# Optimization experiments

Hardware: AMD Instinct MI355X
Metric: run time of the kernel (lower is better)

The kernel has to match this reference:

```python
import jax, jax.numpy as jnp
import numpy as np
from itertools import permutations

NODE, BATCH, DIM, STEP = 32, 64, 32, 8
E = NODE * (NODE - 1)          # 992 directed edges (all ordered pairs)
K = 3                          # edge types
MSG_HID = 64; MSG_OUT = 64; N_HID = 64; PRED_LEN = 8


def setup_inputs() -> dict:
    key = jax.random.key(0)
    ks = jax.random.split(key, 12)
    es = jnp.asarray(np.array(list(permutations(range(NODE), 2))).T, dtype=jnp.int32)  # [2, E]
    x = jax.random.normal(ks[0], (BATCH, NODE, DIM, STEP), jnp.float32)
    z = jax.nn.softmax(jax.random.normal(ks[1], (BATCH, E, K), jnp.float32), axis=-1)
    p = lambda k, shape: jax.random.normal(k, shape, jnp.float32) * 0.1
    return dict(
        x=x, z=z, es=es,
        nodes_mask=jnp.zeros((NODE,), jnp.float32),
        edges_mask=jnp.zeros((E,), jnp.float32),
        mask=jnp.zeros((1,), jnp.float32),
        msg_W1=p(ks[2], (K, 2 * DIM, MSG_HID)), msg_b1=jnp.zeros((K, MSG_HID), jnp.float32),
        msg_W2=p(ks[3], (K, MSG_HID, MSG_OUT)), msg_b2=jnp.zeros((K, MSG_OUT), jnp.float32),
        out_W1=p(ks[4], (DIM + MSG_OUT, N_HID)), out_b1=jnp.zeros((N_HID,), jnp.float32),
        out_W2=p(ks[5], (N_HID, N_HID)), out_b2=jnp.zeros((N_HID,), jnp.float32),
        out_W3=p(ks[6], (N_HID, DIM)), out_b3=jnp.zeros((DIM,), jnp.float32),
        ge_Wi=p(ks[7], (3, N_HID, N_HID)), ge_bi=jnp.zeros((3, N_HID), jnp.float32),
        ge_Wh=p(ks[8], (3, N_HID, N_HID)), ge_bh=jnp.zeros((3, N_HID), jnp.float32),
        gn_Wi=p(ks[9], (3, N_HID + DIM, N_HID + DIM)), gn_bi=jnp.zeros((3, N_HID + DIM), jnp.float32),
        gn_Wh=p(ks[10], (3, N_HID + DIM, N_HID + DIM)), gn_bh=jnp.zeros((3, N_HID + DIM), jnp.float32),
    )


def _gru(inp, hid, Wi, bi, Wh, bh):
    # GRUX: state defaults to hidden
    r = jax.nn.sigmoid(inp @ Wi[0] + bi[0] + hid @ Wh[0] + bh[0])
    i = jax.nn.sigmoid(inp @ Wi[1] + bi[1] + hid @ Wh[1] + bh[1])
    n = jnp.tanh(inp @ Wi[2] + bi[2] + r * (hid @ Wh[2] + bh[2]))
    return (1.0 - i) * n + i * hid


def _run(x, z, es, msg_W1, msg_b1, msg_W2, msg_b2,
         out_W1, out_b1, out_W2, out_b2, out_W3, out_b3,
         ge_Wi, ge_bi, ge_Wh, ge_bh, gn_Wi, gn_bi, gn_Wh, gn_bh):
    xp = jnp.transpose(x, (1, 0, 3, 2))   # [node, batch, step, dim]
    zp = jnp.transpose(z, (1, 0, 2))      # [E, batch, K]
    col, row = es[0], es[1]               # 'o2i': col,row = es; aggregate at col
    counts = jnp.clip(jax.ops.segment_sum(jnp.ones((E,), x.dtype), col, num_segments=NODE), 1.0)
    h_node = h_edge = None
    x_m = None
    xs = []
    for t in range(STEP + PRED_LEN):
        x_in = xp[:, :, t, :] if t < STEP else x_m   # [node, batch, dim]
        # edge gather: msg = cat([x[row], x[col]])
        msg = jnp.concatenate([x_in[row], x_in[col]], axis=-1)  # [E, b, 2*dim]
        # per-edge-type 2-layer MLP mixture, weighted by z, normalized by K
        h1 = jax.nn.relu(jnp.einsum('ebi,kih->kebh', msg, msg_W1) + msg_b1[:, None, None, :])
        h2 = jax.nn.relu(jnp.einsum('kebh,kho->kebo', h1, msg_W2) + msg_b2[:, None, None, :])
        msgs = jnp.einsum('kebo,ebk->ebo', h2, zp) / K          # [E, b, msg_out]
        if h_edge is not None:
            msgs = _gru(msgs, h_edge, ge_Wi, ge_bi, ge_Wh, ge_bh)
        # scatter-mean to nodes
        agg = jax.ops.segment_sum(msgs, col, num_segments=NODE) / counts[:, None, None]
        cat = jnp.concatenate([x_in, agg], axis=-1)             # [node, b, dim+msg_out]
        if h_node is not None:
            cat = _gru(cat, h_node, gn_Wi, gn_bi, gn_Wh, gn_bh)
        h = jax.nn.relu(cat @ out_W1 + out_b1)
        h = jax.nn.relu(h @ out_W2 + out_b2)
        delta = h @ out_W3 + out_b3
        x_m = x_in + delta
        h_node, h_edge = cat, msgs
        xs.append(x_m)
    x_hat = jnp.transpose(jnp.stack(xs, axis=2), (1, 0, 3, 2))  # [batch, node, dim, T]
    return x_hat


def reference(x, z, es, nodes_mask, edges_mask, mask,
              msg_W1, msg_b1, msg_W2, msg_b2,
              out_W1, out_b1, out_W2, out_b2, out_W3, out_b3,
              ge_Wi, ge_bi, ge_Wh, ge_bh, gn_Wi, gn_bi, gn_Wh, gn_bh):
    x_hat = _run(x, z, es, msg_W1, msg_b1, msg_W2, msg_b2,
                 out_W1, out_b1, out_W2, out_b2, out_W3, out_b3,
                 ge_Wi, ge_bi, ge_Wh, ge_bh, gn_Wi, gn_bi, gn_Wh, gn_bh)
    return (x_hat[:, :, :, -PRED_LEN:], x_hat, x_hat)
```

## Files before the change

### kernel.cpp

```cpp
#include <hip/hip_runtime.h>
#include <hip/hip_bf16.h>

#define NNODE 32
#define NB    64
#define NDIM  32
#define NSTEP 8
#define NE    992
#define NTT   16

typedef __bf16 bf16;
typedef __attribute__((ext_vector_type(8))) __bf16 bf16x8;
typedef __attribute__((ext_vector_type(4))) __bf16 bf16x4;
typedef __attribute__((ext_vector_type(4))) float  f32x4;

__device__ __forceinline__ f32x4 mfma_bf16(bf16x8 a, bf16x8 b, f32x4 c) {
  return __builtin_amdgcn_mfma_f32_16x16x32_bf16(a, b, c, 0, 0, 0);
}
__device__ __forceinline__ float sigm(float x) { return 1.0f / (1.0f + __expf(-x)); }
__device__ __forceinline__ float tanh_f(float x) {
  x = fminf(fmaxf(x, -15.0f), 15.0f);
  float e = __expf(2.0f * x);
  return (e - 1.0f) / (e + 1.0f);
}

__global__ void prep_weights(
    const float* __restrict__ msgW1, const float* __restrict__ msgW2,
    const float* __restrict__ geWi,  const float* __restrict__ geWh,
    const float* __restrict__ gnWi,  const float* __restrict__ gnWh,
    const float* __restrict__ oW1,   const float* __restrict__ oW2,
    const float* __restrict__ oW3,
    bf16* __restrict__ B1, bf16* __restrict__ B2,
    bf16* __restrict__ GI, bf16* __restrict__ GH,
    bf16* __restrict__ GN,
    bf16* __restrict__ OW1s, bf16* __restrict__ OW2s, bf16* __restrict__ OW3s) {
  int u = blockIdx.x * 256 + threadIdx.x;
  if (u < 12288) {
    int k = u >> 12, i = (u >> 6) & 63, h = u & 63;
    int kf = i >> 5, quad = (i >> 3) & 3, j = i & 7;
    int nn = k * 64 + h, nt = nn >> 4, lane = quad * 16 + (nn & 15);
    int slot = ((nt * 2 + kf) * 64 + lane) * 8 + j;
    B1[slot] = (bf16)msgW1[u];
    GI[slot] = (bf16)geWi[u];
    GH[slot] = (bf16)geWh[u];
    int ntl = h >> 4, lane2 = quad * 16 + (h & 15);
    int slot2 = k * 4096 + ((ntl * 2 + kf) * 64 + lane2) * 8 + j;
    B2[slot2] = (bf16)msgW2[u];
  } else if (u < 39936) {
    int v = u - 12288;
    int kk = v / 9216, rem = v % 9216, i = rem / 96, h = rem % 96;
    int kf = i >> 5, loc = i & 31, quad = loc >> 3, j = loc & 7;
    int nn = kk * 96 + h, nt = nn >> 4, lane = quad * 16 + (nn & 15);
    int slot = ((nt * 3 + kf) * 64 + lane) * 8 + j;
    GN[slot]         = (bf16)gnWi[v];
    GN[27648 + slot] = (bf16)gnWh[v];
  } else if (u < 46080) {
    int v = u - 39936; int i = v >> 6, h = v & 63;
    int kf = i >> 5, loc = i & 31, quad = loc >> 3, j = loc & 7;
    int nt = h >> 4, lane = quad * 16 + (h & 15);
    OW1s[((nt * 3 + kf) * 64 + lane) * 8 + j] = (bf16)oW1[v];
  } else if (u < 50176) {
    int v = u - 46080; int i = v >> 6, h = v & 63;
    int kf = i >> 5, quad = (i >> 3) & 3, j = i & 7;
    int nt = h >> 4, lane = quad * 16 + (h & 15);
    OW2s[((nt * 2 + kf) * 64 + lane) * 8 + j] = (bf16)oW2[v];
  } else if (u < 52224) {
    int v = u - 50176; int i = v >> 5, h = v & 31;
    int kf = i >> 5, quad = (i >> 3) & 3, j = i & 7;
    int nt = h >> 4, lane = quad * 16 + (h & 15);
    OW3s[((nt * 2 + kf) * 64 + lane) * 8 + j] = (bf16)oW3[v];
  }
}

__global__ void copy_x(const float* __restrict__ x, float* __restrict__ xf,
                       bf16* __restrict__ xb) {
  int u = blockIdx.x * 256 + threadIdx.x;
  int n = u >> 11, b = (u >> 5) & 63, d = u & 31;
  float v = x[((b * 32 + n) * 32 + d) * 8 + 0];
  xf[u] = v;
  xb[u] = (bf16)v;
}

__global__ __launch_bounds__(256, 2) void edge_step(
    const bf16* __restrict__ xb, const int* __restrict__ es,
    const float* __restrict__ z,
    const bf16* __restrict__ B1, const bf16* __restrict__ B2,
    const float* __restrict__ mb1, const float* __restrict__ mb2,
    const bf16* __restrict__ GI, const bf16* __restrict__ GH,
    const float* __restrict__ gbi, const float* __restrict__ gbh,
    bf16* __restrict__ hed, int t) {
  __shared__ __align__(16) char scrbuf[51200];
  __shared__ float zL[2][64][3];
  __shared__ float biasL[768];
  bf16 (*A)[64][72]   = (bf16(*)[64][72])scrbuf;
  bf16 (*A2)[64][200] = (bf16(*)[64][200])scrbuf;

  int e0 = blockIdx.x * 2, tid = threadIdx.x;
  int c0_ = es[e0],     r0 = es[NE + e0];
  int c1_ = es[e0 + 1], r1 = es[NE + e0 + 1];
  for (int u = tid; u < 768; u += 256)
    biasL[u] = (u < 192) ? mb1[u] : (u < 384) ? mb2[u - 192]
             : (u < 576) ? gbi[u - 384] : gbh[u - 576];
  for (int u = tid; u < 384; u += 256) {
    int pe = u / 192, rem = u % 192, b = rem / 3, k = rem % 3;
    zL[pe][b][k] = z[(b * NE + e0 + pe) * 3 + k];
  }
  for (int u = tid; u < 1024; u += 256) {
    int pe = u >> 9, c = u & 511;
    int b = c >> 3, i8 = c & 7;
    int nrow = pe ? r1 : r0, ncol = pe ? c1_ : c0_;
    const bf16* src = (i8 < 4) ? (xb + nrow * 2048 + b * 32 + i8 * 8)
                               : (xb + ncol * 2048 + b * 32 + (i8 - 4) * 8);
    *(bf16x8*)&A[pe][b][i8 * 8] = *(const bf16x8*)src;
  }
  __syncthreads();
  int wv = tid >> 6, ln = tid & 63, quad = ln >> 4, l16 = ln & 15;
  int m = wv * 16 + l16;
  bf16x8 af[2][2];
#pragma unroll
  for (int pe = 0; pe < 2; pe++)
#pragma unroll
    for (int kf = 0; kf < 2; kf++)
      af[pe][kf] = *(const bf16x8*)&A[pe][m][kf * 32 + quad * 8];
  __syncthreads();
  f32x4 acc[2][12];
#pragma unroll
  for (int pe = 0; pe < 2; pe++)
#pragma unroll
    for (int q = 0; q < 12; q++) { f32x4 zz = {0.f,0.f,0.f,0.f}; acc[pe][q] = zz; }
#pragma unroll
  for (int nt = 0; nt < 12; nt++) {
    bf16x8 w0 = *(const bf16x8*)&B1[(nt * 2 + 0) * 512 + ln * 8];
    bf16x8 w1 = *(const bf16x8*)&B1[(nt * 2 + 1) * 512 + ln * 8];
#pragma unroll
    for (int pe = 0; pe < 2; pe++) {
      acc[pe][nt] = mfma_bf16(af[pe][0], w0, acc[pe][nt]);
      acc[pe][nt] = mfma_bf16(af[pe][1], w1, acc[pe][nt]);
    }
  }
#pragma unroll
  for (int nt = 0; nt < 12; nt++) {
    int n = nt * 16 + l16;
    float bias = biasL[n];
#pragma unroll
    for (int pe = 0; pe < 2; pe++)
#pragma unroll
      for (int r = 0; r < 4; r++) {
        float v = acc[pe][nt][r] + bias;
        A2[pe][wv * 16 + quad * 4 + r][n] = (bf16)(v > 0.f ? v : 0.f);
      }
  }
  __syncthreads();
  bf16x8 a2[2][3][2];
#pragma unroll
  for (int pe = 0; pe < 2; pe++)
#pragma unroll
    for (int kt = 0; kt < 3; kt++)
#pragma unroll
      for (int kf = 0; kf < 2; kf++)
        a2[pe][kt][kf] = *(const bf16x8*)&A2[pe][m][kt * 64 + kf * 32 + quad * 8];
  __syncthreads();
  f32x4 acc2[2][12];
#pragma unroll
  for (int pe = 0; pe < 2; pe++)
#pragma unroll
    for (int q = 0; q < 12; q++) { f32x4 zz = {0.f,0.f,0.f,0.f}; acc2[pe][q] = zz; }
#pragma unroll
  for (int kt = 0; kt < 3; kt++)
#pragma unroll
    for (int nt = 0; nt < 4; nt++) {
      bf16x8 w0 = *(const bf16x8*)&B2[kt * 4096 + (nt * 2 + 0) * 512 + ln * 8];
      bf16x8 w1 = *(const bf16x8*)&B2[kt * 4096 + (nt * 2 + 1) * 512 + ln * 8];
#pragma unroll
      for (int pe = 0; pe < 2; pe++) {
        acc2[pe][kt * 4 + nt] = mfma_bf16(a2[pe][kt][0], w0, acc2[pe][kt * 4 + nt]);
        acc2[pe][kt * 4 + nt] = mfma_bf16(a2[pe][kt][1], w1, acc2[pe][kt * 4 + nt]);
      }
    }
#pragma unroll
  for (int pe = 0; pe < 2; pe++)
#pragma unroll
    for (int r = 0; r < 4; r++) {
      int b = wv * 16 + quad * 4 + r;
      float z0 = zL[pe][b][0], z1 = zL[pe][b][1], z2 = zL[pe][b][2];
#pragma unroll
      for (int nt = 0; nt < 4; nt++) {
        int o = nt * 16 + l16;
        float h0 = acc2[pe][nt][r]     + biasL[192 + o];       h0 = h0 > 0.f ? h0 : 0.f;
        float h1 = acc2[pe][4 + nt][r] + biasL[192 + 64 + o];  h1 = h1 > 0.f ? h1 : 0.f;
        float h2 = acc2[pe][8 + nt][r] + biasL[192 + 128 + o]; h2 = h2 > 0.f ? h2 : 0.f;
        A[pe][b][o] = (bf16)((h0 * z0 + h1 * z1 + h2 * z2) * (1.0f / 3.0f));
      }
    }
  if (t > 0) {
    __syncthreads();
    bf16x8 ai[2][2], ah[2][2];
#pragma unroll
    for (int pe = 0; pe < 2; pe++) {
      const bf16* hrow = hed + (e0 + pe) * 4096 + m * 64;
#pragma unroll
      for (int kf = 0; kf < 2; kf++) {
        ai[pe][kf] = *(const bf16x8*)&A[pe][m][kf * 32 + quad * 8];
        ah[pe][kf] = *(const bf16x8*)(hrow + kf * 32 + quad * 8);
      }
    }
    f32x4 gri[2][8], gni[2][4], gnh[2][4];
#pragma unroll
    for (int pe = 0; pe < 2; pe++) {
#pragma unroll
      for (int q = 0; q < 8; q++) { f32x4 zz = {0.f,0.f,0.f,0.f}; gri[pe][q] = zz; }
#pragma unroll
      for (int q = 0; q < 4; q++) { f32x4 zz = {0.f,0.f,0.f,0.f}; gni[pe][q] = zz; gnh[pe][q] = zz; }
    }
#pragma unroll
    for (int nt = 0; nt < 8; nt++) {
      bf16x8 wi0 = *(const bf16x8*)&GI[(nt * 2 + 0) * 512 + ln * 8];
      bf16x8 wi1 = *(const bf16x8*)&GI[(nt * 2 + 1) * 512 + ln * 8];
      bf16x8 wh0 = *(const bf16x8*)&GH[(nt * 2 + 0) * 512 + ln * 8];
      bf16x8 wh1 = *(const bf16x8*)&GH[(nt * 2 + 1) * 512 + ln * 8];
#pragma unroll
      for (int pe = 0; pe < 2; pe++) {
        gri[pe][nt] = mfma_bf16(ai[pe][0], wi0, gri[pe][nt]);
        gri[pe][nt] = mfma_bf16(ai[pe][1], wi1, gri[pe][nt]);
        gri[pe][nt] = mfma_bf16(ah[pe][0], wh0, gri[pe][nt]);
        gri[pe][nt] = mfma_bf16(ah[pe][1], wh1, gri[pe][nt]);
      }
    }
#pragma unroll
    for (int nt = 8; nt < 12; nt++) {
      bf16x8 wi0 = *(const bf16x8*)&GI[(nt * 2 + 0) * 512 + ln * 8];
      bf16x8 wi1 = *(const bf16x8*)&GI[(nt * 2 + 1) * 512 + ln * 8];
      bf16x8 wh0 = *(const bf16x8*)&GH[(nt * 2 + 0) * 512 + ln * 8];
      bf16x8 wh1 = *(const bf16x8*)&GH[(nt * 2 + 1) * 512 + ln * 8];
#pragma unroll
      for (int pe = 0; pe < 2; pe++) {
        gni[pe][nt - 8] = mfma_bf16(ai[pe][0], wi0, gni[pe][nt - 8]);
        gni[pe][nt - 8] = mfma_bf16(ai[pe][1], wi1, gni[pe][nt - 8]);
        gnh[pe][nt - 8] = mfma_bf16(ah[pe][0], wh0, gnh[pe][nt - 8]);
        gnh[pe][nt - 8] = mfma_bf16(ah[pe][1], wh1, gnh[pe][nt - 8]);
      }
    }
#pragma unroll
    for (int pe = 0; pe < 2; pe++)
#pragma unroll
      for (int r = 0; r < 4; r++) {
        int b = wv * 16 + quad * 4 + r;
#pragma unroll
        for (int nt = 0; nt < 4; nt++) {
          int o = nt * 16 + l16;
          float xr = gri[pe][nt][r]     + biasL[384 + o]      + biasL[576 + o];
          float xi = gri[pe][4 + nt][r] + biasL[384 + 64 + o] + biasL[576 + 64 + o];
          float xn = gni[pe][nt][r] + biasL[384 + 128 + o];
          float hn = gnh[pe][nt][r] + biasL[576 + 128 + o];
          float rg = sigm(xr);
          float ig = sigm(xi);
          float ng = tanh_f(xn + rg * hn);
          float hv = (float)hed[(e0 + pe) * 4096 + b * 64 + o];
          A[pe][b][o] = (bf16)((1.0f - ig) * ng + ig * hv);
        }
      }
  }
  __syncthreads();
  for (int u = tid; u < 1024; u += 256) {
    int pe = u >> 9, c = u & 511;
    int b = c >> 3, j = c & 7;
    *(bf16x8*)(hed + (e0 + pe) * 4096 + b * 64 + j * 8) = *(const bf16x8*)&A[pe][b][j * 8];
  }
}

__global__ __launch_bounds__(256) void node_kernel(
    const float* __restrict__ x, const bf16* __restrict__ hed,
    float* __restrict__ xf, bf16* __restrict__ xb, float* __restrict__ hnode,
    const bf16* __restrict__ GN,
    const float* __restrict__ gnbi, const float* __restrict__ gnbh,
    const bf16* __restrict__ OW1, const float* __restrict__ ob1,
    const bf16* __restrict__ OW2, const float* __restrict__ ob2,
    const bf16* __restrict__ OW3, const float* __restrict__ ob3,
    float* __restrict__ out, int t) {
  __shared__ float aggf[16][64];
  __shared__ float xinf[16][32];
  __shared__ float hvf[16][96];
  __shared__ __align__(16) bf16 c0b[16][112];
  __shared__ __align__(16) bf16 hvb[16][112];
  __shared__ float gsum[2][16][290];
  __shared__ __align__(16) bf16 cnb[16][112];
  __shared__ __align__(16) bf16 s1b[16][112];
  __shared__ __align__(16) bf16 s2b[16][112];
  int nq = blockIdx.x, n = nq >> 2, q = nq & 3;
  int tid = threadIdx.x;
  {
    int r = tid >> 4, o4 = tid & 15;
    const bf16x4* bp = (const bf16x4*)hed + (size_t)n * 31 * 1024 + (q * 16 + r) * 16 + o4;
    float sx = 0.f, sy = 0.f, sz = 0.f, sw = 0.f;
#pragma unroll
    for (int e2 = 0; e2 < 31; e2++) {
      bf16x4 v = bp[e2 * 1024];
      sx += (float)v[0]; sy += (float)v[1]; sz += (float)v[2]; sw += (float)v[3];
    }
    const float inv = 1.0f / 31.0f;
    sx *= inv; sy *= inv; sz *= inv; sw *= inv;
    int o = o4 * 4;
    aggf[r][o] = sx; aggf[r][o + 1] = sy; aggf[r][o + 2] = sz; aggf[r][o + 3] = sw;
    c0b[r][32 + o] = (bf16)sx; c0b[r][33 + o] = (bf16)sy;
    c0b[r][34 + o] = (bf16)sz; c0b[r][35 + o] = (bf16)sw;
  }
  if (tid < 128) {
    int r = tid >> 3, d0 = (tid & 7) * 4;
    int b = q * 16 + r;
#pragma unroll
    for (int k = 0; k < 4; k++) {
      float v = xf[n * 2048 + b * 32 + d0 + k];
      xinf[r][d0 + k] = v;
      c0b[r][d0 + k] = (bf16)v;
    }
  }
  if (t > 0) {
    int r = tid >> 4, cb = (tid & 15) * 6;
    int row = n * 64 + q * 16 + r;
#pragma unroll
    for (int k = 0; k < 6; k++) {
      float v = hnode[row * 96 + cb + k];
      hvf[r][cb + k] = v;
      hvb[r][cb + k] = (bf16)v;
    }
  }
  __syncthreads();
  int wv = tid >> 6, ln = tid & 63, quad = ln >> 4, l16 = ln & 15;
  if (t > 0) {
    int mat = wv >> 1, sel = wv & 1;
    const bf16(*Ab)[112] = mat ? hvb : c0b;
    bf16x8 af[3];
#pragma unroll
    for (int kf = 0; kf < 3; kf++)
      af[kf] = *(const bf16x8*)&Ab[l16][kf * 32 + quad * 8];
    const bf16* W = GN + mat * 27648;
    f32x4 accn[9];
#pragma unroll
    for (int q2 = 0; q2 < 9; q2++) { f32x4 zz = {0.f,0.f,0.f,0.f}; accn[q2] = zz; }
#pragma unroll
    for (int nt2 = 0; nt2 < 9; nt2++) {
      int nt = sel * 9 + nt2;
#pragma unroll
      for (int kf = 0; kf < 3; kf++) {
        bf16x8 bfrag = *(const bf16x8*)&W[((nt * 3 + kf) * 64 + ln) * 8];
        accn[nt2] = mfma_bf16(af[kf], bfrag, accn[nt2]);
      }
    }
#pragma unroll
    for (int nt2 = 0; nt2 < 9; nt2++) {
      int col = (sel * 9 + nt2) * 16 + l16;
#pragma unroll
      for (int rr = 0; rr < 4; rr++)
        gsum[mat][quad * 4 + rr][col] = accn[nt2][rr];
    }
  }
  __syncthreads();
  {
    int r = tid >> 4, cb = (tid & 15) * 6;
    int row = n * 64 + q * 16 + r;
#pragma unroll
    for (int k = 0; k < 6; k++) {
      int c = cb + k;
      float v;
      if (t > 0) {
        float xr = gsum[0][r][c] + gnbi[c] + gsum[1][r][c] + gnbh[c];
        float xi = gsum[0][r][96 + c] + gnbi[96 + c] + gsum[1][r][96 + c] + gnbh[96 + c];
        float xn = gsum[0][r][192 + c] + gnbi[192 + c];
        float hn = gsum[1][r][192 + c] + gnbh[192 + c];
        float rg = sigm(xr);
        float ig = sigm(xi);
        float ng = tanh_f(xn + rg * hn);
        v = (1.0f - ig) * ng + ig * hvf[r][c];
      } else {
        v = (c < 32) ? xinf[r][c] : aggf[r][c - 32];
      }
      cnb[r][c] = (bf16)v;
      hnode[row * 96 + c] = v;
    }
  }
  __syncthreads();
  {
    bf16x8 af[3];
#pragma unroll
    for (int kf = 0; kf < 3; kf++)
      af[kf] = *(const bf16x8*)&cnb[l16][kf * 32 + quad * 8];
    f32x4 accn = {0.f, 0.f, 0.f, 0.f};
#pragma unroll
    for (int kf = 0; kf < 3; kf++) {
      bf16x8 bfrag = *(const bf16x8*)&OW1[((wv * 3 + kf) * 64 + ln) * 8];
      accn = mfma_bf16(af[kf], bfrag, accn);
    }
    int col = wv * 16 + l16;
    float bias = ob1[col];
#pragma unroll
    for (int rr = 0; rr < 4; rr++) {
      float vv = accn[rr] + bias;
      s1b[quad * 4 + rr][col] = (bf16)(vv > 0.f ? vv : 0.f);
    }
  }
  __syncthreads();
  {
    bf16x8 af[2];
#pragma unroll
    for (int kf = 0; kf < 2; kf++)
      af[kf] = *(const bf16x8*)&s1b[l16][kf * 32 + quad * 8];
    f32x4 accn = {0.f, 0.f, 0.f, 0.f};
#pragma unroll
    for (int kf = 0; kf < 2; kf++) {
      bf16x8 bfrag = *(const bf16x8*)&OW2[((wv * 2 + kf) * 64 + ln) * 8];
      accn = mfma_bf16(af[kf], bfrag, accn);
    }
    int col = wv * 16 + l16;
    float bias = ob2[col];
#pragma unroll
    for (int rr = 0; rr < 4; rr++) {
      float vv = accn[rr] + bias;
      s2b[quad * 4 + rr][col] = (bf16)(vv > 0.f ? vv : 0.f);
    }
  }
  __syncthreads();
  if (wv < 2) {
    bf16x8 af[2];
#pragma unroll
    for (int kf = 0; kf < 2; kf++)
      af[kf] = *(const bf16x8*)&s2b[l16][kf * 32 + quad * 8];
    f32x4 accn = {0.f, 0.f, 0.f, 0.f};
#pragma unroll
    for (int kf = 0; kf < 2; kf++) {
      bf16x8 bfrag = *(const bf16x8*)&OW3[((wv * 2 + kf) * 64 + ln) * 8];
      accn = mfma_bf16(af[kf], bfrag, accn);
    }
    int d = wv * 16 + l16;
    float bias = ob3[d];
#pragma unroll
    for (int rr = 0; rr < 4; rr++) {
      int r = quad * 4 + rr;
      int b = q * 16 + r;
      float xm = xinf[r][d] + accn[rr] + bias;
      int base = (b * 32 + n) * 32 + d;
      out[524288 + base * 16 + t] = xm;
      out[1572864 + base * 16 + t] = xm;
      if (t >= NSTEP) out[base * 8 + (t - NSTEP)] = xm;
      float vnext = (t + 1 < NSTEP) ? x[base * 8 + (t + 1)] : xm;
      xf[n * 2048 + b * 32 + d] = vnext;
      xb[n * 2048 + b * 32 + d] = (bf16)vnext;
    }
  }
}

extern "C" void kernel_launch(void* const* d_in, const int* in_sizes, int n_in,
                              void* d_out, int out_size, void* d_ws, size_t ws_size,
                              hipStream_t stream) {
  const float* x     = (const float*)d_in[0];
  const float* z     = (const float*)d_in[1];
  const int*   es    = (const int*)d_in[2];
  const float* msgW1 = (const float*)d_in[6];
  const float* msgb1 = (const float*)d_in[7];
  const float* msgW2 = (const float*)d_in[8];
  const float* msgb2 = (const float*)d_in[9];
  const float* oW1   = (const float*)d_in[10];
  const float* ob1   = (const float*)d_in[11];
  const float* oW2   = (const float*)d_in[12];
  const float* ob2   = (const float*)d_in[13];
  const float* oW3   = (const float*)d_in[14];
  const float* ob3   = (const float*)d_in[15];
  const float* geWi  = (const float*)d_in[16];
  const float* gebi  = (const float*)d_in[17];
  const float* geWh  = (const float*)d_in[18];
  const float* gebh  = (const float*)d_in[19];
  const float* gnWi  = (const float*)d_in[20];
  const float* gnbi  = (const float*)d_in[21];
  const float* gnWh  = (const float*)d_in[22];
  const float* gnbh  = (const float*)d_in[23];
  float* out = (float*)d_out;

  char* p = (char*)d_ws;
  bf16*  hed   = (bf16*)p;   p += (size_t)NE * 4096 * 2;
  float* xf    = (float*)p;  p += 65536 * 4;
  bf16*  xb    = (bf16*)p;   p += 65536 * 2;
  float* hnode = (float*)p;  p += 196608 * 4;
  bf16*  B1sw  = (bf16*)p;   p += 12288 * 2;
  bf16*  B2sw  = (bf16*)p;   p += 12288 * 2;
  bf16*  GIsw  = (bf16*)p;   p += 12288 * 2;
  bf16*  GHsw  = (bf16*)p;   p += 12288 * 2;
  bf16*  GNsw  = (bf16*)p;   p += 55296 * 2;
  bf16*  OW1s  = (bf16*)p;   p += 6144 * 2;
  bf16*  OW2s  = (bf16*)p;   p += 4096 * 2;
  bf16*  OW3s  = (bf16*)p;   p += 2048 * 2;

  prep_weights<<<204, 256, 0, stream>>>(msgW1, msgW2, geWi, geWh, gnWi, gnWh,
                                        oW1, oW2, oW3,
                                        B1sw, B2sw, GIsw, GHsw, GNsw,
                                        OW1s, OW2s, OW3s);
  copy_x<<<256, 256, 0, stream>>>(x, xf, xb);

  for (int t = 0; t < NTT; t++) {
    edge_step<<<NE / 2, 256, 0, stream>>>(xb, es, z, B1sw, B2sw, msgb1, msgb2,
                                          GIsw, GHsw, gebi, gebh, hed, t);
    node_kernel<<<128, 256, 0, stream>>>(x, hed, xf, xb, hnode, GNsw, gnbi, gnbh,
                                         OW1s, ob1, OW2s, ob2, OW3s, ob3,
                                         out, t);
  }
}
```

Before: 658.2 us.

## Factor first message layer per node and batch teacher-forced steps upfront

Splits the first message-MLP matmul by linearity into per-node projections (receiver and sender halves of W1), computed once per node rather than once per edge. For the teacher-forced steps the inputs are known in advance, so all of them are projected and mixed in two large batched kernels, leaving only the GRU update in the per-step loop. For autoregressive steps the node kernel computes the next-step projection itself. This removes redundant per-edge first-layer MFMAs and exposes more parallelism early, at the cost of large fp32 projection and mixed-message buffers in workspace and extra global traffic to read them.

```diff
diff --git a/kernel.cpp b/kernel.cpp
--- a/kernel.cpp
+++ b/kernel.cpp
@@ -29,7 +29,7 @@
     const float* __restrict__ gnWi,  const float* __restrict__ gnWh,
     const float* __restrict__ oW1,   const float* __restrict__ oW2,
     const float* __restrict__ oW3,
-    bf16* __restrict__ B1, bf16* __restrict__ B2,
+    bf16* __restrict__ W1P, bf16* __restrict__ B2,
     bf16* __restrict__ GI, bf16* __restrict__ GH,
     bf16* __restrict__ GN,
     bf16* __restrict__ OW1s, bf16* __restrict__ OW2s, bf16* __restrict__ OW3s) {
@@ -39,12 +39,15 @@
     int kf = i >> 5, quad = (i >> 3) & 3, j = i & 7;
     int nn = k * 64 + h, nt = nn >> 4, lane = quad * 16 + (nn & 15);
     int slot = ((nt * 2 + kf) * 64 + lane) * 8 + j;
-    B1[slot] = (bf16)msgW1[u];
     GI[slot] = (bf16)geWi[u];
     GH[slot] = (bf16)geWh[u];
     int ntl = h >> 4, lane2 = quad * 16 + (h & 15);
     int slot2 = k * 4096 + ((ntl * 2 + kf) * 64 + lane2) * 8 + j;
     B2[slot2] = (bf16)msgW2[u];
+    int loc = i & 31, q3 = loc >> 3, j3 = loc & 7;
+    int nt3 = kf * 12 + (nn >> 4);
+    int lane3 = q3 * 16 + (nn & 15);
+    W1P[(nt3 * 64 + lane3) * 8 + j3] = (bf16)msgW1[u];
   } else if (u < 39936) {
     int v = u - 12288;
     int kk = v / 9216, rem = v % 9216, i = rem / 96, h = rem % 96;
@@ -71,32 +74,222 @@
   }
 }
 
-__global__ void copy_x(const float* __restrict__ x, float* __restrict__ xf,
-                       bf16* __restrict__ xb) {
+__global__ void copy_x0(const float* __restrict__ x, float* __restrict__ xf) {
   int u = blockIdx.x * 256 + threadIdx.x;
   int n = u >> 11, b = (u >> 5) & 63, d = u & 31;
-  float v = x[((b * 32 + n) * 32 + d) * 8 + 0];
-  xf[u] = v;
-  xb[u] = (bf16)v;
-}
-
-__global__ __launch_bounds__(256, 2) void edge_step(
-    const bf16* __restrict__ xb, const int* __restrict__ es,
+  xf[u] = x[((b * 32 + n) * 32 + d) * 8 + 0];
+}
+
+__global__ __launch_bounds__(256) void p8_kernel(
+    const float* __restrict__ x, const bf16* __restrict__ W1P,
+    float* __restrict__ Pbuf) {
+  __shared__ __align__(16) bf16 XA[64][40];
+  int t = blockIdx.x >> 5, n = blockIdx.x & 31;
+  int tid = threadIdx.x;
+  for (int u = tid; u < 2048; u += 256) {
+    int b = u >> 5, d = u & 31;
+    XA[b][d] = (bf16)x[((b * 32 + n) * 32 + d) * 8 + t];
+  }
+  __syncthreads();
+  int wv = tid >> 6, ln = tid & 63, quad = ln >> 4, l16 = ln & 15;
+  bf16x8 a = *(const bf16x8*)&XA[wv * 16 + l16][quad * 8];
+  float* Pt = Pbuf + ((size_t)(t * 32 + n) * 64) * 384;
+#pragma unroll
+  for (int nt = 0; nt < 24; nt++) {
+    bf16x8 bfr = *(const bf16x8*)&W1P[(nt * 64 + ln) * 8];
+    f32x4 c = {0.f, 0.f, 0.f, 0.f};
+    c = mfma_bf16(a, bfr, c);
+#pragma unroll
+    for (int rr = 0; rr < 4; rr++)
+      Pt[(size_t)(wv * 16 + quad * 4 + rr) * 384 + nt * 16 + l16] = c[rr];
+  }
+}
+
+__device__ __forceinline__ bf16x8 mk_h1(const float* b1p, const float* b2p,
+                                        const float* biasL, int col) {
+  f32x4 pa0 = *(const f32x4*)(b1p + col);
+  f32x4 pa1 = *(const f32x4*)(b1p + col + 4);
+  f32x4 pb0 = *(const f32x4*)(b2p + col);
+  f32x4 pb1 = *(const f32x4*)(b2p + col + 4);
+  bf16x8 h;
+#pragma unroll
+  for (int j = 0; j < 4; j++) {
+    float v0 = pa0[j] + pb0[j] + biasL[col + j];
+    float v1 = pa1[j] + pb1[j] + biasL[col + 4 + j];
+    h[j]     = (bf16)(v0 > 0.f ? v0 : 0.f);
+    h[4 + j] = (bf16)(v1 > 0.f ? v1 : 0.f);
+  }
+  return h;
+}
+
+__global__ __launch_bounds__(256, 2) void mix8_kernel(
+    const float* __restrict__ Pbuf, const int* __restrict__ es,
     const float* __restrict__ z,
-    const bf16* __restrict__ B1, const bf16* __restrict__ B2,
+    const bf16* __restrict__ B2,
+    const float* __restrict__ mb1, const float* __restrict__ mb2,
+    bf16* __restrict__ hed, bf16* __restrict__ mixbuf) {
+  __shared__ float zL[2][64][3];
+  __shared__ float biasL[384];
+  int t = blockIdx.x / 496, pair = blockIdx.x % 496;
+  int e0 = pair * 2, tid = threadIdx.x;
+  int cn0 = es[e0], rn0 = es[NE + e0];
+  int cn1 = es[e0 + 1], rn1 = es[NE + e0 + 1];
+  for (int u = tid; u < 384; u += 256)
+    biasL[u] = (u < 192) ? mb1[u] : mb2[u - 192];
+  for (int u = tid; u < 384; u += 256) {
+    int pe = u / 192, rem = u % 192, b = rem / 3, k = rem % 3;
+    zL[pe][b][k] = z[(b * NE + e0 + pe) * 3 + k];
+  }
+  __syncthreads();
+  int wv = tid >> 6, ln = tid & 63, quad = ln >> 4, l16 = ln & 15;
+  int m = wv * 16 + l16;
+  bf16x8 a2[2][3][2];
+#pragma unroll
+  for (int pe = 0; pe < 2; pe++) {
+    int rn = pe ? rn1 : rn0, cnn = pe ? cn1 : cn0;
+    const float* b1p = Pbuf + ((size_t)(t * 32 + rn) * 64 + m) * 384;
+    const float* b2p = Pbuf + ((size_t)(t * 32 + cnn) * 64 + m) * 384 + 192;
+#pragma unroll
+    for (int kt = 0; kt < 3; kt++)
+#pragma unroll
+      for (int kf = 0; kf < 2; kf++)
+        a2[pe][kt][kf] = mk_h1(b1p, b2p, biasL, kt * 64 + kf * 32 + quad * 8);
+  }
+  f32x4 acc2[2][12];
+#pragma unroll
+  for (int pe = 0; pe < 2; pe++)
+#pragma unroll
+    for (int q = 0; q < 12; q++) { f32x4 zz = {0.f,0.f,0.f,0.f}; acc2[pe][q] = zz; }
+#pragma unroll
+  for (int kt = 0; kt < 3; kt++)
+#pragma unroll
+    for (int nt = 0; nt < 4; nt++) {
+      bf16x8 w0 = *(const bf16x8*)&B2[kt * 4096 + (nt * 2 + 0) * 512 + ln * 8];
+      bf16x8 w1 = *(const bf16x8*)&B2[kt * 4096 + (nt * 2 + 1) * 512 + ln * 8];
+#pragma unroll
+      for (int pe = 0; pe < 2; pe++) {
+        acc2[pe][kt * 4 + nt] = mfma_bf16(a2[pe][kt][0], w0, acc2[pe][kt * 4 + nt]);
+        acc2[pe][kt * 4 + nt] = mfma_bf16(a2[pe][kt][1], w1, acc2[pe][kt * 4 + nt]);
+      }
+    }
+#pragma unroll
+  for (int pe = 0; pe < 2; pe++) {
+    bf16* dst = (t == 0) ? (hed + (size_t)(e0 + pe) * 4096)
+                         : (mixbuf + ((size_t)(t - 1) * NE + e0 + pe) * 4096);
+#pragma unroll
+    for (int r = 0; r < 4; r++) {
+      int b = wv * 16 + quad * 4 + r;
+      float z0 = zL[pe][b][0], z1 = zL[pe][b][1], z2 = zL[pe][b][2];
+#pragma unroll
+      for (int nt = 0; nt < 4; nt++) {
+        int o = nt * 16 + l16;
+        float h0 = acc2[pe][nt][r]     + biasL[192 + o];       h0 = h0 > 0.f ? h0 : 0.f;
+        float h1 = acc2[pe][4 + nt][r] + biasL[192 + 64 + o];  h1 = h1 > 0.f ? h1 : 0.f;
+        float h2 = acc2[pe][8 + nt][r] + biasL[192 + 128 + o]; h2 = h2 > 0.f ? h2 : 0.f;
+        dst[b * 64 + o] = (bf16)((h0 * z0 + h1 * z1 + h2 * z2) * (1.0f / 3.0f));
+      }
+    }
+  }
+}
+
+__global__ __launch_bounds__(256, 2) void gru_step(
+    const bf16* __restrict__ mixbuf, bf16* __restrict__ hed,
+    const bf16* __restrict__ GI, const bf16* __restrict__ GH,
+    const float* __restrict__ gbi, const float* __restrict__ gbh, int t) {
+  __shared__ __align__(16) bf16 S[2][64][72];
+  __shared__ float gb[384];
+  int e0 = blockIdx.x * 2, tid = threadIdx.x;
+  for (int u = tid; u < 384; u += 256)
+    gb[u] = (u < 192) ? gbi[u] : gbh[u - 192];
+  int wv = tid >> 6, ln = tid & 63, quad = ln >> 4, l16 = ln & 15;
+  int m = wv * 16 + l16;
+  bf16x8 ai[2][2], ah[2][2];
+#pragma unroll
+  for (int pe = 0; pe < 2; pe++) {
+    const bf16* mrow = mixbuf + ((size_t)(t - 1) * NE + e0 + pe) * 4096 + m * 64;
+    const bf16* hrow = hed + (size_t)(e0 + pe) * 4096 + m * 64;
+#pragma unroll
+    for (int kf = 0; kf < 2; kf++) {
+      ai[pe][kf] = *(const bf16x8*)(mrow + kf * 32 + quad * 8);
+      ah[pe][kf] = *(const bf16x8*)(hrow + kf * 32 + quad * 8);
+    }
+  }
+  f32x4 gri[2][8], gni[2][4], gnh[2][4];
+#pragma unroll
+  for (int pe = 0; pe < 2; pe++) {
+#pragma unroll
+    for (int q = 0; q < 8; q++) { f32x4 zz = {0.f,0.f,0.f,0.f}; gri[pe][q] = zz; }
+#pragma unroll
+    for (int q = 0; q < 4; q++) { f32x4 zz = {0.f,0.f,0.f,0.f}; gni[pe][q] = zz; gnh[pe][q] = zz; }
+  }
+#pragma unroll
+  for (int nt = 0; nt < 8; nt++) {
+    bf16x8 wi0 = *(const bf16x8*)&GI[(nt * 2 + 0) * 512 + ln * 8];
+    bf16x8 wi1 = *(const bf16x8*)&GI[(nt * 2 + 1) * 512 + ln * 8];
+    bf16x8 wh0 = *(const bf16x8*)&GH[(nt * 2 + 0) * 512 + ln * 8];
+    bf16x8 wh1 = *(const bf16x8*)&GH[(nt * 2 + 1) * 512 + ln * 8];
+#pragma unroll
+    for (int pe = 0; pe < 2; pe++) {
+      gri[pe][nt] = mfma_bf16(ai[pe][0], wi0, gri[pe][nt]);
+      gri[pe][nt] = mfma_bf16(ai[pe][1], wi1, gri[pe][nt]);
+      gri[pe][nt] = mfma_bf16(ah[pe][0], wh0, gri[pe][nt]);
+      gri[pe][nt] = mfma_bf16(ah[pe][1], wh1, gri[pe][nt]);
+    }
+  }
+#pragma unroll
+  for (int nt = 8; nt < 12; nt++) {
+    bf16x8 wi0 = *(const bf16x8*)&GI[(nt * 2 + 0) * 512 + ln * 8];
+    bf16x8 wi1 = *(const bf16x8*)&GI[(nt * 2 + 1) * 512 + ln * 8];
+    bf16x8 wh0 = *(const bf16x8*)&GH[(nt * 2 + 0) * 512 + ln * 8];
+    bf16x8 wh1 = *(const bf16x8*)&GH[(nt * 2 + 1) * 512 + ln * 8];
+#pragma unroll
+    for (int pe = 0; pe < 2; pe++) {
+      gni[pe][nt - 8] = mfma_bf16(ai[pe][0], wi0, gni[pe][nt - 8]);
+      gni[pe][nt - 8] = mfma_bf16(ai[pe][1], wi1, gni[pe][nt - 8]);
+      gnh[pe][nt - 8] = mfma_bf16(ah[pe][0], wh0, gnh[pe][nt - 8]);
+      gnh[pe][nt - 8] = mfma_bf16(ah[pe][1], wh1, gnh[pe][nt - 8]);
+    }
+  }
+#pragma unroll
+  for (int pe = 0; pe < 2; pe++)
+#pragma unroll
+    for (int r = 0; r < 4; r++) {
+      int b = wv * 16 + quad * 4 + r;
+#pragma unroll
+      for (int nt = 0; nt < 4; nt++) {
+        int o = nt * 16 + l16;
+        float xr = gri[pe][nt][r]     + gb[o]      + gb[192 + o];
+        float xi = gri[pe][4 + nt][r] + gb[64 + o] + gb[192 + 64 + o];
+        float xn = gni[pe][nt][r] + gb[128 + o];
+        float hn = gnh[pe][nt][r] + gb[192 + 128 + o];
+        float rg = sigm(xr);
+        float ig = sigm(xi);
+        float ng = tanh_f(xn + rg * hn);
+        float hv = (float)hed[(size_t)(e0 + pe) * 4096 + b * 64 + o];
+        S[pe][b][o] = (bf16)((1.0f - ig) * ng + ig * hv);
+      }
+    }
+  __syncthreads();
+  for (int u = tid; u < 1024; u += 256) {
+    int pe = u >> 9, c = u & 511, b = c >> 3, j = c & 7;
+    *(bf16x8*)(hed + (size_t)(e0 + pe) * 4096 + b * 64 + j * 8) = *(const bf16x8*)&S[pe][b][j * 8];
+  }
+}
+
+__global__ __launch_bounds__(256, 2) void edge_full(
+    const float* __restrict__ Pcur, const int* __restrict__ es,
+    const float* __restrict__ z,
+    const bf16* __restrict__ B2,
     const float* __restrict__ mb1, const float* __restrict__ mb2,
     const bf16* __restrict__ GI, const bf16* __restrict__ GH,
     const float* __restrict__ gbi, const float* __restrict__ gbh,
-    bf16* __restrict__ hed, int t) {
-  __shared__ __align__(16) char scrbuf[51200];
+    bf16* __restrict__ hed) {
+  __shared__ __align__(16) bf16 S[2][64][72];
   __shared__ float zL[2][64][3];
   __shared__ float biasL[768];
-  bf16 (*A)[64][72]   = (bf16(*)[64][72])scrbuf;
-  bf16 (*A2)[64][200] = (bf16(*)[64][200])scrbuf;
-
   int e0 = blockIdx.x * 2, tid = threadIdx.x;
-  int c0_ = es[e0],     r0 = es[NE + e0];
-  int c1_ = es[e0 + 1], r1 = es[NE + e0 + 1];
+  int cn0 = es[e0], rn0 = es[NE + e0];
+  int cn1 = es[e0 + 1], rn1 = es[NE + e0 + 1];
   for (int u = tid; u < 768; u += 256)
     biasL[u] = (u < 192) ? mb1[u] : (u < 384) ? mb2[u - 192]
              : (u < 576) ? gbi[u - 384] : gbh[u - 576];
@@ -104,61 +297,21 @@
     int pe = u / 192, rem = u % 192, b = rem / 3, k = rem % 3;
     zL[pe][b][k] = z[(b * NE + e0 + pe) * 3 + k];
   }
-  for (int u = tid; u < 1024; u += 256) {
-    int pe = u >> 9, c = u & 511;
-    int b = c >> 3, i8 = c & 7;
-    int nrow = pe ? r1 : r0, ncol = pe ? c1_ : c0_;
-    const bf16* src = (i8 < 4) ? (xb + nrow * 2048 + b * 32 + i8 * 8)
-                               : (xb + ncol * 2048 + b * 32 + (i8 - 4) * 8);
-    *(bf16x8*)&A[pe][b][i8 * 8] = *(const bf16x8*)src;
-  }
   __syncthreads();
   int wv = tid >> 6, ln = tid & 63, quad = ln >> 4, l16 = ln & 15;
   int m = wv * 16 + l16;
-  bf16x8 af[2][2];
-#pragma unroll
-  for (int pe = 0; pe < 2; pe++)
-#pragma unroll
-    for (int kf = 0; kf < 2; kf++)
-      af[pe][kf] = *(const bf16x8*)&A[pe][m][kf * 32 + quad * 8];
-  __syncthreads();
-  f32x4 acc[2][12];
-#pragma unroll
-  for (int pe = 0; pe < 2; pe++)
-#pragma unroll
-    for (int q = 0; q < 12; q++) { f32x4 zz = {0.f,0.f,0.f,0.f}; acc[pe][q] = zz; }
-#pragma unroll
-  for (int nt = 0; nt < 12; nt++) {
-    bf16x8 w0 = *(const bf16x8*)&B1[(nt * 2 + 0) * 512 + ln * 8];
-    bf16x8 w1 = *(const bf16x8*)&B1[(nt * 2 + 1) * 512 + ln * 8];
-#pragma unroll
-    for (int pe = 0; pe < 2; pe++) {
-      acc[pe][nt] = mfma_bf16(af[pe][0], w0, acc[pe][nt]);
-      acc[pe][nt] = mfma_bf16(af[pe][1], w1, acc[pe][nt]);
-    }
-  }
-#pragma unroll
-  for (int nt = 0; nt < 12; nt++) {
-    int n = nt * 16 + l16;
-    float bias = biasL[n];
-#pragma unroll
-    for (int pe = 0; pe < 2; pe++)
-#pragma unroll
-      for (int r = 0; r < 4; r++) {
-        float v = acc[pe][nt][r] + bias;
-        A2[pe][wv * 16 + quad * 4 + r][n] = (bf16)(v > 0.f ? v : 0.f);
-      }
-  }
-  __syncthreads();
   bf16x8 a2[2][3][2];
 #pragma unroll
-  for (int pe = 0; pe < 2; pe++)
+  for (int pe = 0; pe < 2; pe++) {
+    int rn = pe ? rn1 : rn0, cnn = pe ? cn1 : cn0;
+    const float* b1p = Pcur + ((size_t)rn * 64 + m) * 384;
+    const float* b2p = Pcur + ((size_t)cnn * 64 + m) * 384 + 192;
 #pragma unroll
     for (int kt = 0; kt < 3; kt++)
 #pragma unroll
       for (int kf = 0; kf < 2; kf++)
-        a2[pe][kt][kf] = *(const bf16x8*)&A2[pe][m][kt * 64 + kf * 32 + quad * 8];
-  __syncthreads();
+        a2[pe][kt][kf] = mk_h1(b1p, b2p, biasL, kt * 64 + kf * 32 + quad * 8);
+  }
   f32x4 acc2[2][12];
 #pragma unroll
   for (int pe = 0; pe < 2; pe++)
@@ -188,93 +341,91 @@
         float h0 = acc2[pe][nt][r]     + biasL[192 + o];       h0 = h0 > 0.f ? h0 : 0.f;
         float h1 = acc2[pe][4 + nt][r] + biasL[192 + 64 + o];  h1 = h1 > 0.f ? h1 : 0.f;
         float h2 = acc2[pe][8 + nt][r] + biasL[192 + 128 + o]; h2 = h2 > 0.f ? h2 : 0.f;
-        A[pe][b][o] = (bf16)((h0 * z0 + h1 * z1 + h2 * z2) * (1.0f / 3.0f));
-      }
-    }
-  if (t > 0) {
-    __syncthreads();
-    bf16x8 ai[2][2], ah[2][2];
+        S[pe][b][o] = (bf16)((h0 * z0 + h1 * z1 + h2 * z2) * (1.0f / 3.0f));
+      }
+    }
+  __syncthreads();
+  bf16x8 ai[2][2], ah[2][2];
+#pragma unroll
+  for (int pe = 0; pe < 2; pe++) {
+    const bf16* hrow = hed + (size_t)(e0 + pe) * 4096 + m * 64;
+#pragma unroll
+    for (int kf = 0; kf < 2; kf++) {
+      ai[pe][kf] = *(const bf16x8*)&S[pe][m][kf * 32 + quad * 8];
+      ah[pe][kf] = *(const bf16x8*)(hrow + kf * 32 + quad * 8);
+    }
+  }
+  f32x4 gri[2][8], gni[2][4], gnh[2][4];
+#pragma unroll
+  for (int pe = 0; pe < 2; pe++) {
+#pragma unroll
+    for (int q = 0; q < 8; q++) { f32x4 zz = {0.f,0.f,0.f,0.f}; gri[pe][q] = zz; }
+#pragma unroll
+    for (int q = 0; q < 4; q++) { f32x4 zz = {0.f,0.f,0.f,0.f}; gni[pe][q] = zz; gnh[pe][q] = zz; }
+  }
+#pragma unroll
+  for (int nt = 0; nt < 8; nt++) {
+    bf16x8 wi0 = *(const bf16x8*)&GI[(nt * 2 + 0) * 512 + ln * 8];
+    bf16x8 wi1 = *(const bf16x8*)&GI[(nt * 2 + 1) * 512 + ln * 8];
+    bf16x8 wh0 = *(const bf16x8*)&GH[(nt * 2 + 0) * 512 + ln * 8];
+    bf16x8 wh1 = *(const bf16x8*)&GH[(nt * 2 + 1) * 512 + ln * 8];
 #pragma unroll
     for (int pe = 0; pe < 2; pe++) {
-      const bf16* hrow = hed + (e0 + pe) * 4096 + m * 64;
-#pragma unroll
-      for (int kf = 0; kf < 2; kf++) {
-        ai[pe][kf] = *(const bf16x8*)&A[pe][m][kf * 32 + quad * 8];
-        ah[pe][kf] = *(const bf16x8*)(hrow + kf * 32 + quad * 8);
-      }
-    }
-    f32x4 gri[2][8], gni[2][4], gnh[2][4];
+      gri[pe][nt] = mfma_bf16(ai[pe][0], wi0, gri[pe][nt]);
+      gri[pe][nt] = mfma_bf16(ai[pe][1], wi1, gri[pe][nt]);
+      gri[pe][nt] = mfma_bf16(ah[pe][0], wh0, gri[pe][nt]);
+      gri[pe][nt] = mfma_bf16(ah[pe][1], wh1, gri[pe][nt]);
+    }
+  }
+#pragma unroll
+  for (int nt = 8; nt < 12; nt++) {
+    bf16x8 wi0 = *(const bf16x8*)&GI[(nt * 2 + 0) * 512 + ln * 8];
+    bf16x8 wi1 = *(const bf16x8*)&GI[(nt * 2 + 1) * 512 + ln * 8];
+    bf16x8 wh0 = *(const bf16x8*)&GH[(nt * 2 + 0) * 512 + ln * 8];
+    bf16x8 wh1 = *(const bf16x8*)&GH[(nt * 2 + 1) * 512 + ln * 8];
 #pragma unroll
     for (int pe = 0; pe < 2; pe++) {
-#pragma unroll
-      for (int q = 0; q < 8; q++) { f32x4 zz = {0.f,0.f,0.f,0.f}; gri[pe][q] = zz; }
-#pragma unroll
-      for (int q = 0; q < 4; q++) { f32x4 zz = {0.f,0.f,0.f,0.f}; gni[pe][q] = zz; gnh[pe][q] = zz; }
-    }
-#pragma unroll
-    for (int nt = 0; nt < 8; nt++) {
-      bf16x8 wi0 = *(const bf16x8*)&GI[(nt * 2 + 0) * 512 + ln * 8];
-      bf16x8 wi1 = *(const bf16x8*)&GI[(nt * 2 + 1) * 512 + ln * 8];
-      bf16x8 wh0 = *(const bf16x8*)&GH[(nt * 2 + 0) * 512 + ln * 8];
-      bf16x8 wh1 = *(const bf16x8*)&GH[(nt * 2 + 1) * 512 + ln * 8];
-#pragma unroll
-      for (int pe = 0; pe < 2; pe++) {
-        gri[pe][nt] = mfma_bf16(ai[pe][0], wi0, gri[pe][nt]);
-        gri[pe][nt] = mfma_bf16(ai[pe][1], wi1, gri[pe][nt]);
-        gri[pe][nt] = mfma_bf16(ah[pe][0], wh0, gri[pe][nt]);
-        gri[pe][nt] = mfma_bf16(ah[pe][1], wh1, gri[pe][nt]);
-      }
-    }
-#pragma unroll
-    for (int nt = 8; nt < 12; nt++) {
-      bf16x8 wi0 = *(const bf16x8*)&GI[(nt * 2 + 0) * 512 + ln * 8];
-      bf16x8 wi1 = *(const bf16x8*)&GI[(nt * 2 + 1) * 512 + ln * 8];
-      bf16x8 wh0 = *(const bf16x8*)&GH[(nt * 2 + 0) * 512 + ln * 8];
-      bf16x8 wh1 = *(const bf16x8*)&GH[(nt * 2 + 1) * 512 + ln * 8];
-#pragma unroll
-      for (int pe = 0; pe < 2; pe++) {
-        gni[pe][nt - 8] = mfma_bf16(ai[pe][0], wi0, gni[pe][nt - 8]);
-        gni[pe][nt - 8] = mfma_bf16(ai[pe][1], wi1, gni[pe][nt - 8]);
-        gnh[pe][nt - 8] = mfma_bf16(ah[pe][0], wh0, gnh[pe][nt - 8]);
-        gnh[pe][nt - 8] = mfma_bf16(ah[pe][1], wh1, gnh[pe][nt - 8]);
-      }
-    }
-#pragma unroll
-    for (int pe = 0; pe < 2; pe++)
-#pragma unroll
-      for (int r = 0; r < 4; r++) {
-        int b = wv * 16 + quad * 4 + r;
-#pragma unroll
-        for (int nt = 0; nt < 4; nt++) {
-          int o = nt * 16 + l16;
-          float xr = gri[pe][nt][r]     + biasL[384 + o]      + biasL[576 + o];
-          float xi = gri[pe][4 + nt][r] + biasL[384 + 64 + o] + biasL[576 + 64 + o];
-          float xn = gni[pe][nt][r] + biasL[384 + 128 + o];
-          float hn = gnh[pe][nt][r] + biasL[576 + 128 + o];
-          float rg = sigm(xr);
-          float ig = sigm(xi);
-          float ng = tanh_f(xn + rg * hn);
-          float hv = (float)hed[(e0 + pe) * 4096 + b * 64 + o];
-          A[pe][b][o] = (bf16)((1.0f - ig) * ng + ig * hv);
-        }
-      }
-  }
+      gni[pe][nt - 8] = mfma_bf16(ai[pe][0], wi0, gni[pe][nt - 8]);
+      gni[pe][nt - 8] = mfma_bf16(ai[pe][1], wi1, gni[pe][nt - 8]);
+      gnh[pe][nt - 8] = mfma_bf16(ah[pe][0], wh0, gnh[pe][nt - 8]);
+      gnh[pe][nt - 8] = mfma_bf16(ah[pe][1], wh1, gnh[pe][nt - 8]);
+    }
+  }
+#pragma unroll
+  for (int pe = 0; pe < 2; pe++)
+#pragma unroll
+    for (int r = 0; r < 4; r++) {
+      int b = wv * 16 + quad * 4 + r;
+#pragma unroll
+      for (int nt = 0; nt < 4; nt++) {
+        int o = nt * 16 + l16;
+        float xr = gri[pe][nt][r]     + biasL[384 + o]      + biasL[576 + o];
+        float xi = gri[pe][4 + nt][r] + biasL[384 + 64 + o] + biasL[576 + 64 + o];
+        float xn = gni[pe][nt][r] + biasL[384 + 128 + o];
+        float hn = gnh[pe][nt][r] + biasL[576 + 128 + o];
+        float rg = sigm(xr);
+        float ig = sigm(xi);
+        float ng = tanh_f(xn + rg * hn);
+        float hv = (float)hed[(size_t)(e0 + pe) * 4096 + b * 64 + o];
+        S[pe][b][o] = (bf16)((1.0f - ig) * ng + ig * hv);
+      }
+    }
   __syncthreads();
   for (int u = tid; u < 1024; u += 256) {
-    int pe = u >> 9, c = u & 511;
-    int b = c >> 3, j = c & 7;
-    *(bf16x8*)(hed + (e0 + pe) * 4096 + b * 64 + j * 8) = *(const bf16x8*)&A[pe][b][j * 8];
+    int pe = u >> 9, c = u & 511, b = c >> 3, j = c & 7;
+    *(bf16x8*)(hed + (size_t)(e0 + pe) * 4096 + b * 64 + j * 8) = *(const bf16x8*)&S[pe][b][j * 8];
   }
 }
 
 __global__ __launch_bounds__(256) void node_kernel(
     const float* __restrict__ x, const bf16* __restrict__ hed,
-    float* __restrict__ xf, bf16* __restrict__ xb, float* __restrict__ hnode,
+    float* __restrict__ xf, float* __restrict__ hnode,
     const bf16* __restrict__ GN,
     const float* __restrict__ gnbi, const float* __restrict__ gnbh,
     const bf16* __restrict__ OW1, const float* __restrict__ ob1,
     const bf16* __restrict__ OW2, const float* __restrict__ ob2,
     const bf16* __restrict__ OW3, const float* __restrict__ ob3,
+    const bf16* __restrict__ W1P, float* __restrict__ Pcur,
     float* __restrict__ out, int t) {
   __shared__ float aggf[16][64];
   __shared__ float xinf[16][32];
@@ -285,6 +436,7 @@
   __shared__ __align__(16) bf16 cnb[16][112];
   __shared__ __align__(16) bf16 s1b[16][112];
   __shared__ __align__(16) bf16 s2b[16][112];
+  __shared__ __align__(16) bf16 xnb[16][40];
   int nq = blockIdx.x, n = nq >> 2, q = nq & 3;
   int tid = threadIdx.x;
   {
@@ -442,7 +594,21 @@
       if (t >= NSTEP) out[base * 8 + (t - NSTEP)] = xm;
       float vnext = (t + 1 < NSTEP) ? x[base * 8 + (t + 1)] : xm;
       xf[n * 2048 + b * 32 + d] = vnext;
-      xb[n * 2048 + b * 32 + d] = (bf16)vnext;
+      xnb[r][d] = (bf16)vnext;
+    }
+  }
+  __syncthreads();
+  if (t + 1 >= NSTEP && t + 1 < NTT) {
+    bf16x8 a = *(const bf16x8*)&xnb[l16][quad * 8];
+#pragma unroll
+    for (int s = 0; s < 6; s++) {
+      int nt = wv * 6 + s;
+      bf16x8 bfr = *(const bf16x8*)&W1P[(nt * 64 + ln) * 8];
+      f32x4 c = {0.f, 0.f, 0.f, 0.f};
+      c = mfma_bf16(a, bfr, c);
+#pragma unroll
+      for (int rr = 0; rr < 4; rr++)
+        Pcur[(size_t)(n * 64 + q * 16 + quad * 4 + rr) * 384 + nt * 16 + l16] = c[rr];
     }
   }
 }
@@ -475,10 +641,12 @@
 
   char* p = (char*)d_ws;
   bf16*  hed   = (bf16*)p;   p += (size_t)NE * 4096 * 2;
+  bf16*  mixbuf= (bf16*)p;   p += (size_t)7 * NE * 4096 * 2;
+  float* Pbuf  = (float*)p;  p += (size_t)8 * 32 * 64 * 384 * 4;
+  float* Pcur  = (float*)p;  p += (size_t)32 * 64 * 384 * 4;
   float* xf    = (float*)p;  p += 65536 * 4;
-  bf16*  xb    = (bf16*)p;   p += 65536 * 2;
   float* hnode = (float*)p;  p += 196608 * 4;
-  bf16*  B1sw  = (bf16*)p;   p += 12288 * 2;
+  bf16*  W1Psw = (bf16*)p;   p += 12288 * 2;
   bf16*  B2sw  = (bf16*)p;   p += 12288 * 2;
   bf16*  GIsw  = (bf16*)p;   p += 12288 * 2;
   bf16*  GHsw  = (bf16*)p;   p += 12288 * 2;
@@ -489,15 +657,26 @@
 
   prep_weights<<<204, 256, 0, stream>>>(msgW1, msgW2, geWi, geWh, gnWi, gnWh,
                                         oW1, oW2, oW3,
-                                        B1sw, B2sw, GIsw, GHsw, GNsw,
+                                        W1Psw, B2sw, GIsw, GHsw, GNsw,
                                         OW1s, OW2s, OW3s);
-  copy_x<<<256, 256, 0, stream>>>(x, xf, xb);
-
-  for (int t = 0; t < NTT; t++) {
-    edge_step<<<NE / 2, 256, 0, stream>>>(xb, es, z, B1sw, B2sw, msgb1, msgb2,
-                                          GIsw, GHsw, gebi, gebh, hed, t);
-    node_kernel<<<128, 256, 0, stream>>>(x, hed, xf, xb, hnode, GNsw, gnbi, gnbh,
+  copy_x0<<<256, 256, 0, stream>>>(x, xf);
+  p8_kernel<<<256, 256, 0, stream>>>(x, W1Psw, Pbuf);
+  mix8_kernel<<<8 * 496, 256, 0, stream>>>(Pbuf, es, z, B2sw, msgb1, msgb2,
+                                           hed, mixbuf);
+  node_kernel<<<128, 256, 0, stream>>>(x, hed, xf, hnode, GNsw, gnbi, gnbh,
+                                       OW1s, ob1, OW2s, ob2, OW3s, ob3,
+                                       W1Psw, Pcur, out, 0);
+  for (int t = 1; t < NSTEP; t++) {
+    gru_step<<<496, 256, 0, stream>>>(mixbuf, hed, GIsw, GHsw, gebi, gebh, t);
+    node_kernel<<<128, 256, 0, stream>>>(x, hed, xf, hnode, GNsw, gnbi, gnbh,
                                          OW1s, ob1, OW2s, ob2, OW3s, ob3,
-                                         out, t);
-  }
-}
+                                         W1Psw, Pcur, out, t);
+  }
+  for (int t = NSTEP; t < NTT; t++) {
+    edge_full<<<496, 256, 0, stream>>>(Pcur, es, z, B2sw, msgb1, msgb2,
+                                       GIsw, GHsw, gebi, gebh, hed);
+    node_kernel<<<128, 256, 0, stream>>>(x, hed, xf, hnode, GNsw, gnbi, gnbh,
+                                         OW1s, ob1, OW2s, ob2, OW3s, ob3,
+                                         W1Psw, Pcur, out, t);
+  }
+}
```

After: 847.6 us. 28.8% more time.
